# Performance work log

Hardware: AMD Instinct MI355X
Metric: run time of the kernel (lower is better)

Reference implementation:

```python
import jax, jax.numpy as jnp
import numpy as np

HIDDEN = 2048
HEADS = 16
HEAD_DIM = HIDDEN // HEADS          # 128
KV_RANK = HIDDEN // 8               # 256 (kv_compression_ratio = 8)
ATTN_DIM = HEADS * HEAD_DIM         # 2048
EPS = 1e-6


def setup_inputs() -> dict:
    key = jax.random.key(0)
    ks = jax.random.split(key, 6)
    B, L = 2, 2048
    x = jax.random.normal(ks[0], (B, L, HIDDEN), dtype=jnp.float32)
    # weights stored [in, out] (torch Linear applies x @ W.T; same math)
    s = lambda fan_in: 1.0 / np.sqrt(fan_in)
    Wq = jax.random.normal(ks[1], (HIDDEN, ATTN_DIM), dtype=jnp.float32) * s(HIDDEN)
    Wkv_down = jax.random.normal(ks[2], (HIDDEN, KV_RANK), dtype=jnp.float32) * s(HIDDEN)
    kv_norm_w = jnp.ones((KV_RANK,), dtype=jnp.float32)
    Wkv_up = jax.random.normal(ks[3], (KV_RANK, 2 * ATTN_DIM), dtype=jnp.float32) * s(KV_RANK)
    Wo = jax.random.normal(ks[4], (ATTN_DIM, HIDDEN), dtype=jnp.float32) * s(ATTN_DIM)
    return {"x": x, "Wq": Wq, "Wkv_down": Wkv_down, "kv_norm_w": kv_norm_w,
            "Wkv_up": Wkv_up, "Wo": Wo}


def rms_norm(x, w):
    ms = jnp.mean(x * x, axis=-1, keepdims=True)
    return w * (x * jax.lax.rsqrt(ms + EPS))


def reference(x, Wq, Wkv_down, kv_norm_w, Wkv_up, Wo):
    B, L, D = x.shape
    q = (x @ Wq).reshape(B, L, HEADS, HEAD_DIM)
    latent = rms_norm(x @ Wkv_down, kv_norm_w)            # [B, L, KV_RANK]
    kv = latent @ Wkv_up                                   # [B, L, 2*ATTN_DIM]
    k, v = jnp.split(kv, 2, axis=-1)
    k = k.reshape(B, L, HEADS, HEAD_DIM)
    v = v.reshape(B, L, HEADS, HEAD_DIM)
    scores = jnp.einsum('bxhd,byhd->bhxy', q, k) / np.sqrt(HEAD_DIM)
    causal = jnp.tril(jnp.ones((L, L), dtype=bool))
    scores = jnp.where(causal, scores, -jnp.inf)
    attn = jax.nn.softmax(scores, axis=-1)
    out = jnp.einsum('bhxy,byhd->bxhd', attn, v).reshape(B, L, ATTN_DIM)
    return out @ Wo
```

## Files before the change

kernel.cpp:

```cpp
#include <hip/hip_runtime.h>
#include <cstdint>
#include <cstddef>

typedef unsigned short u16;
typedef __bf16 bf16x8 __attribute__((ext_vector_type(8)));
typedef __bf16 bf16x2 __attribute__((ext_vector_type(2)));
typedef float f32x4 __attribute__((ext_vector_type(4)));

__device__ inline u16 f2bf(float f) {
  uint32_t u = __builtin_bit_cast(uint32_t, f);
  u += 0x7fffu + ((u >> 16) & 1u);
  return (u16)(u >> 16);
}

#if defined(__has_builtin)
#if __has_builtin(__builtin_amdgcn_cvt_pk_bf16_f32)
#define HAVE_PK_BF16 1
#endif
#endif

__device__ inline uint32_t pk2bf(float a, float b) {
#ifdef HAVE_PK_BF16
  bf16x2 v = __builtin_amdgcn_cvt_pk_bf16_f32(a, b);
  return __builtin_bit_cast(uint32_t, v);
#else
  return (uint32_t)f2bf(a) | ((uint32_t)f2bf(b) << 16);
#endif
}

__device__ inline f32x4 mfma16(bf16x8 a, bf16x8 b, f32x4 c) {
  return __builtin_amdgcn_mfma_f32_16x16x32_bf16(a, b, c, 0, 0, 0);
}

__device__ inline void gl_lds16(const u16* g, u16* l) {
  __builtin_amdgcn_global_load_lds(
      (const __attribute__((address_space(1))) uint32_t*)g,
      (__attribute__((address_space(3))) uint32_t*)l, 16, 0, 0);
}

__device__ void tcvt_dev(const float* __restrict__ in, u16* __restrict__ out,
                         int R, int C, int bx, int by, float (*t)[33], int tid) {
  int cb = bx * 32, rb = by * 32;
  int x = tid & 31, y = tid >> 5;
#pragma unroll
  for (int k = 0; k < 4; ++k)
    t[y + k * 8][x] = in[(size_t)(rb + y + k * 8) * C + cb + x];
  __syncthreads();
#pragma unroll
  for (int k = 0; k < 4; ++k)
    out[(size_t)(cb + y + k * 8) * R + rb + x] = f2bf(t[x][y + k * 8]);
}

__global__ __launch_bounds__(256) void k_prep(
    const float* __restrict__ x, const float* __restrict__ Wq,
    const float* __restrict__ Wkvd, const float* __restrict__ Wkvu,
    const float* __restrict__ Wo, u16* __restrict__ xbf,
    u16* __restrict__ WqkdT, u16* __restrict__ WkvuT, u16* __restrict__ WoT) {
  __shared__ float t[32][33];
  int bid = blockIdx.x, tid = threadIdx.x;
  if (bid < 8192) {
    int i = bid * 256 + tid;
    const float4 v = ((const float4*)x)[i];
    ushort4 o;
    o.x = f2bf(v.x); o.y = f2bf(v.y); o.z = f2bf(v.z); o.w = f2bf(v.w);
    ((ushort4*)xbf)[i] = o;
  } else if (bid < 12288) {
    int q = bid - 8192;
    tcvt_dev(Wq, WqkdT, 2048, 2048, q & 63, q >> 6, t, tid);
  } else if (bid < 12800) {
    int q = bid - 12288;
    tcvt_dev(Wkvd, WqkdT + 2048 * 2048, 2048, 256, q & 7, q >> 3, t, tid);
  } else if (bid < 13824) {
    int q = bid - 12800;
    tcvt_dev(Wkvu, WkvuT, 256, 4096, q & 127, q >> 7, t, tid);
  } else {
    int q = bid - 13824;
    tcvt_dev(Wo, WoT, 2048, 2048, q & 63, q >> 6, t, tid);
  }
}

__global__ __launch_bounds__(256) void k_rmsn(const u16* __restrict__ qc,
                                              const float* __restrict__ w,
                                              u16* __restrict__ out) {
  int row = blockIdx.x * 4 + (threadIdx.x >> 6);
  int lane = threadIdx.x & 63;
  const ushort4 u = *(const ushort4*)(qc + (size_t)row * 2304 + 2048 + lane * 4);
  float4 v;
  v.x = __builtin_bit_cast(float, (uint32_t)u.x << 16);
  v.y = __builtin_bit_cast(float, (uint32_t)u.y << 16);
  v.z = __builtin_bit_cast(float, (uint32_t)u.z << 16);
  v.w = __builtin_bit_cast(float, (uint32_t)u.w << 16);
  float ss = v.x * v.x + v.y * v.y + v.z * v.z + v.w * v.w;
#pragma unroll
  for (int off = 1; off < 64; off <<= 1) ss += __shfl_xor(ss, off);
  float r = rsqrtf(ss * (1.f / 256.f) + 1e-6f);
  const float4 wv = ((const float4*)w)[lane];
  ushort4 o;
  o.x = f2bf(v.x * r * wv.x);
  o.y = f2bf(v.y * r * wv.y);
  o.z = f2bf(v.z * r * wv.z);
  o.w = f2bf(v.w * r * wv.w);
  *(ushort4*)(out + (size_t)row * 256 + lane * 4) = o;
}

template <int BK, int MODE>
__global__ __launch_bounds__(256) void k_gemm(const u16* __restrict__ A,
                                              const u16* __restrict__ BT,
                                              void* __restrict__ C,
                                              u16* __restrict__ C2, int K,
                                              int ldc, float scale) {
  __shared__ __align__(16) u16 As[128 * BK];
  __shared__ __align__(16) u16 Bs[128 * BK];
  const int tid = threadIdx.x, wave = tid >> 6, lane = tid & 63;
  const int lanem = lane & 15, quad = lane >> 4;
  const int m0 = blockIdx.x * 128, n0 = blockIdx.y * 128;
  const int wr = wave >> 1, wc = wave & 1;
  f32x4 acc[4][4] = {};
  for (int k0 = 0; k0 < K; k0 += BK) {
    __syncthreads();
    if constexpr (BK == 32) {
      const int srow = lane >> 2, scol = (lane & 3) * 8;
#pragma unroll
      for (int c = 0; c < 2; ++c) {
        int p = wave * 2 + c;
        gl_lds16(A + (size_t)(m0 + p * 16 + srow) * K + k0 + scol, &As[p * 512]);
        gl_lds16(BT + (size_t)(n0 + p * 16 + srow) * K + k0 + scol, &Bs[p * 512]);
      }
    } else {
      const int srow = lane >> 3;
      const int scol = ((lane & 7) ^ srow) * 8;
#pragma unroll
      for (int c = 0; c < 4; ++c) {
        int p = wave * 4 + c;
        gl_lds16(A + (size_t)(m0 + p * 8 + srow) * K + k0 + scol, &As[p * 512]);
        gl_lds16(BT + (size_t)(n0 + p * 8 + srow) * K + k0 + scol, &Bs[p * 512]);
      }
    }
    __syncthreads();
#pragma unroll
    for (int kk = 0; kk < BK / 32; ++kk) {
      bf16x8 af[4], bff[4];
      if constexpr (BK == 32) {
#pragma unroll
        for (int i = 0; i < 4; ++i)
          af[i] = *(const bf16x8*)&As[(wr * 64 + i * 16 + lanem) * 32 + quad * 8];
#pragma unroll
        for (int j = 0; j < 4; ++j)
          bff[j] = *(const bf16x8*)&Bs[(wc * 64 + j * 16 + lanem) * 32 + quad * 8];
      } else {
        const int kp = ((kk * 4 + quad) ^ (lanem & 7)) << 3;
#pragma unroll
        for (int i = 0; i < 4; ++i)
          af[i] = *(const bf16x8*)&As[(wr * 64 + i * 16 + lanem) * 64 + kp];
#pragma unroll
        for (int j = 0; j < 4; ++j)
          bff[j] = *(const bf16x8*)&Bs[(wc * 64 + j * 16 + lanem) * 64 + kp];
      }
#pragma unroll
      for (int i = 0; i < 4; ++i)
#pragma unroll
        for (int j = 0; j < 4; ++j)
          acc[i][j] = mfma16(af[i], bff[j], acc[i][j]);
    }
  }
#pragma unroll
  for (int i = 0; i < 4; ++i)
#pragma unroll
    for (int j = 0; j < 4; ++j) {
      const int row0 = m0 + wr * 64 + i * 16 + quad * 4;
      const int col = n0 + wc * 64 + j * 16 + lanem;
      if constexpr (MODE == 2) {
        if (col >= 2048) {
          int cc = col - 2048, hh = cc >> 7, dd = cc & 127;
          int bb = row0 >> 11, ll = row0 & 2047;
          ushort4 pk;
          pk.x = f2bf(acc[i][j][0]);
          pk.y = f2bf(acc[i][j][1]);
          pk.z = f2bf(acc[i][j][2]);
          pk.w = f2bf(acc[i][j][3]);
          *(ushort4*)&C2[((size_t)(bb * 16 + hh) * 128 + dd) * 2048 + ll] = pk;
          continue;
        }
      }
#pragma unroll
      for (int r = 0; r < 4; ++r) {
        float v = acc[i][j][r] * scale;
        if constexpr (MODE == 0)
          ((float*)C)[(size_t)(row0 + r) * ldc + col] = v;
        else if constexpr (MODE == 1)
          ((u16*)C)[(size_t)(row0 + r) * ldc + col] = f2bf(v);
        else
          ((u16*)C)[(size_t)(row0 + r) * 2048 + col] = f2bf(v);
      }
    }
}

__global__ __launch_bounds__(256) void k_attn(const u16* __restrict__ qg,
                                              const u16* __restrict__ kg,
                                              const u16* __restrict__ vtg,
                                              u16* __restrict__ ao) {
  __shared__ __align__(16) u16 Ks[2][64 * 128];
  __shared__ __align__(16) u16 VTs[2][144 * 64];
  __shared__ __align__(16) u16 Ps[4][16 * 64];
  const int bid = blockIdx.x;
  const int p = bid >> 5, u = bid & 31;
  const int qt = (bid < 256) ? (15 - p) : (p - 8);
  const int bh = (u & 7) * 4 + (u >> 3);
  const int b = bh >> 4, h = bh & 15;
  const int tid = threadIdx.x, w = tid >> 6, lane = tid & 63;
  const int lanem = lane & 15, quad = lane >> 4;
  const int qb = qt * 128, nt = 2 * qt + 2;

  const int kr = lane >> 4, kc = lane & 15;
  const u16* kbp[4];
#pragma unroll
  for (int j = 0; j < 4; ++j) {
    int row = w * 16 + j * 4 + kr;
    kbp[j] = kg + (size_t)(b * 2048 + row) * 2048 + h * 128 +
             ((kc ^ (row & 15)) << 3);
  }
  const int vr = lane >> 3, vc = lane & 7;
  const u16* vbp[4];
#pragma unroll
  for (int j = 0; j < 4; ++j) {
    int row = w * 32 + j * 8 + vr;
    vbp[j] = vtg + (size_t)(bh * 128 + row) * 2048 + ((vc ^ vr) << 3);
  }

  bf16x8 qf[2][4];
#pragma unroll
  for (int g = 0; g < 2; ++g) {
    const u16* qp = qg +
                    (size_t)(b * 2048 + qb + w * 32 + g * 16 + lanem) * 2304 +
                    h * 128 + quad * 8;
#pragma unroll
    for (int c = 0; c < 4; ++c) qf[g][c] = *(const bf16x8*)(qp + c * 32);
  }
  f32x4 o[2][9] = {};

  int kpc[4], vposc[2], paddr[4][4];
#pragma unroll
  for (int c = 0; c < 4; ++c) kpc[c] = ((c * 4 + quad) ^ lanem) << 3;
#pragma unroll
  for (int kk = 0; kk < 2; ++kk)
    vposc[kk] = ((kk * 4 + quad) ^ (lanem & 7)) << 3;
#pragma unroll
  for (int ss = 0; ss < 4; ++ss) {
    const int g2 = ss * 2 + (lanem >> 3);
#pragma unroll
    for (int r = 0; r < 4; ++r) {
      const int row = quad * 4 + r;
      paddr[ss][r] = row * 64 + ((g2 ^ (row & 7)) << 3) + (lanem & 7);
    }
  }
  const int prd0 = lanem * 64 + ((quad ^ (lanem & 7)) << 3);
  const int prd1 = lanem * 64 + (((4 + quad) ^ (lanem & 7)) << 3);

#pragma unroll
  for (int j = 0; j < 4; ++j) gl_lds16(kbp[j], &Ks[0][(w * 16 + j * 4) * 128]);
#pragma unroll
  for (int j = 0; j < 4; ++j) gl_lds16(vbp[j], &VTs[0][(w * 32 + j * 8) * 64]);
#pragma unroll
  for (int j = 0; j < 4; ++j) { kbp[j] += 64 * 2048; vbp[j] += 64; }
  {
    const ushort4 ones4{0x3f80u, 0x3f80u, 0x3f80u, 0x3f80u};
    for (int i = tid; i < 512; i += 256) {
      int bufi = i >> 8, off = (i & 255) * 4;
      *(ushort4*)&VTs[bufi][128 * 64 + off] = ones4;
    }
  }

  for (int t = 0; t < nt; ++t) {
    __syncthreads();
    if (t + 1 < nt) {
      int nb = (t + 1) & 1;
#pragma unroll
      for (int j = 0; j < 4; ++j)
        gl_lds16(kbp[j], &Ks[nb][(w * 16 + j * 4) * 128]);
#pragma unroll
      for (int j = 0; j < 4; ++j)
        gl_lds16(vbp[j], &VTs[nb][(w * 32 + j * 8) * 64]);
#pragma unroll
      for (int j = 0; j < 4; ++j) { kbp[j] += 64 * 2048; vbp[j] += 64; }
    }
    const int buf = t & 1;
    const u16* ksb = &Ks[buf][lanem * 128];
    const u16* vsb = &VTs[buf][lanem * 64];
    f32x4 s[2][4] = {};
#pragma unroll
    for (int c = 0; c < 4; ++c) {
      const u16* ka = ksb + kpc[c];
#pragma unroll
      for (int ss = 0; ss < 4; ++ss) {
        bf16x8 kf = *(const bf16x8*)(ka + ss * 2048);
        s[0][ss] = mfma16(qf[0][c], kf, s[0][ss]);
        s[1][ss] = mfma16(qf[1][c], kf, s[1][ss]);
      }
    }
    if (t >= nt - 2) {
      const int krel = t * 64 - qb;
#pragma unroll
      for (int g = 0; g < 2; ++g) {
        const int row = w * 32 + g * 16 + quad * 4;
#pragma unroll
        for (int ss = 0; ss < 4; ++ss)
#pragma unroll
          for (int r = 0; r < 4; ++r)
            if (krel + ss * 16 + lanem > row + r) s[g][ss][r] = -1e30f;
      }
    }
    bf16x8 pf[2][2];
#pragma unroll
    for (int g = 0; g < 2; ++g) {
#pragma unroll
      for (int sp = 0; sp < 2; ++sp)
#pragma unroll
        for (int r = 0; r < 4; ++r) {
          uint32_t pk = pk2bf(exp2f(s[g][sp * 2][r]), exp2f(s[g][sp * 2 + 1][r]));
          Ps[w][paddr[sp * 2][r]] = (u16)pk;
          Ps[w][paddr[sp * 2 + 1][r]] = (u16)(pk >> 16);
        }
      pf[g][0] = *(const bf16x8*)&Ps[w][prd0];
      pf[g][1] = *(const bf16x8*)&Ps[w][prd1];
    }
#pragma unroll
    for (int dc = 0; dc < 9; ++dc) {
      const u16* va = vsb + dc * 1024;
      bf16x8 vf0 = *(const bf16x8*)(va + vposc[0]);
      bf16x8 vf1 = *(const bf16x8*)(va + vposc[1]);
      o[0][dc] = mfma16(pf[0][0], vf0, o[0][dc]);
      o[0][dc] = mfma16(pf[0][1], vf1, o[0][dc]);
      o[1][dc] = mfma16(pf[1][0], vf0, o[1][dc]);
      o[1][dc] = mfma16(pf[1][1], vf1, o[1][dc]);
    }
  }
#pragma unroll
  for (int g = 0; g < 2; ++g)
#pragma unroll
    for (int r = 0; r < 4; ++r) {
      const float inv = 1.f / o[g][8][r];
      u16* op = ao +
                (size_t)(b * 2048 + qb + w * 32 + g * 16 + quad * 4 + r) * 2048 +
                h * 128;
#pragma unroll
      for (int dc = 0; dc < 8; ++dc)
        op[dc * 16 + lanem] = f2bf(o[g][dc][r] * inv);
    }
}

extern "C" void kernel_launch(void* const* d_in, const int* in_sizes, int n_in,
                              void* d_out, int out_size, void* d_ws, size_t ws_size,
                              hipStream_t stream) {
  const float* x    = (const float*)d_in[0];
  const float* Wq   = (const float*)d_in[1];
  const float* Wkvd = (const float*)d_in[2];
  const float* wn   = (const float*)d_in[3];
  const float* Wkvu = (const float*)d_in[4];
  const float* Wo   = (const float*)d_in[5];
  float* out = (float*)d_out;

  char* w0 = (char*)d_ws;
  u16* xbf   = (u16*)(w0);
  u16* qc    = (u16*)(w0 + 16777216);
  u16* WqkdT = (u16*)(w0 + 35651584);
  u16* WoT   = (u16*)(w0 + 45088768);
  u16* WkvuT = (u16*)(w0 + 53477376);
  u16* kbf   = (u16*)(w0 + 55574528);
  u16* vtbf  = (u16*)(w0 + 72351744);
  u16* latbf = WqkdT;
  u16* aobf  = xbf;

  const float sc2 = 0.08838834764831845f * 1.4426950408889634f;

  k_prep<<<17920, 256, 0, stream>>>(x, Wq, Wkvd, Wkvu, Wo, xbf, WqkdT, WkvuT, WoT);
  k_gemm<32, 1><<<dim3(32, 18), 256, 0, stream>>>(xbf, WqkdT, qc, nullptr, 2048,
                                                  2304, sc2);
  k_rmsn<<<1024, 256, 0, stream>>>(qc, wn, latbf);
  k_gemm<64, 2><<<dim3(32, 32), 256, 0, stream>>>(latbf, WkvuT, kbf, vtbf, 256,
                                                  0, 1.0f);
  k_attn<<<512, 256, 0, stream>>>(qc, kbf, vtbf, aobf);
  k_gemm<32, 0><<<dim3(32, 16), 256, 0, stream>>>(aobf, WoT, out, nullptr, 2048,
                                                  2048, 1.0f);
}
```

Measured before the change: 327.1 us.

## Compute transposed S tiles to feed P directly from registers, drop LDS round-trip

After: 314.3 us. -3.9%, faster.

```diff
diff --git a/kernel.cpp b/kernel.cpp
--- a/kernel.cpp
+++ b/kernel.cpp
@@ -6,6 +6,7 @@
 typedef __bf16 bf16x8 __attribute__((ext_vector_type(8)));
 typedef __bf16 bf16x2 __attribute__((ext_vector_type(2)));
 typedef float f32x4 __attribute__((ext_vector_type(4)));
+typedef uint32_t u32x4 __attribute__((ext_vector_type(4)));
 
 __device__ inline u16 f2bf(float f) {
   uint32_t u = __builtin_bit_cast(uint32_t, f);
@@ -17,6 +18,12 @@
 #if __has_builtin(__builtin_amdgcn_cvt_pk_bf16_f32)
 #define HAVE_PK_BF16 1
 #endif
+#if __has_builtin(__builtin_amdgcn_exp2f)
+#define EXP2(x) __builtin_amdgcn_exp2f(x)
+#endif
+#endif
+#ifndef EXP2
+#define EXP2(x) exp2f(x)
 #endif
 
 __device__ inline uint32_t pk2bf(float a, float b) {
@@ -201,7 +208,6 @@
                                               u16* __restrict__ ao) {
   __shared__ __align__(16) u16 Ks[2][64 * 128];
   __shared__ __align__(16) u16 VTs[2][144 * 64];
-  __shared__ __align__(16) u16 Ps[4][16 * 64];
   const int bid = blockIdx.x;
   const int p = bid >> 5, u = bid & 31;
   const int qt = (bid < 256) ? (15 - p) : (p - 8);
@@ -215,9 +221,9 @@
   const u16* kbp[4];
 #pragma unroll
   for (int j = 0; j < 4; ++j) {
-    int row = w * 16 + j * 4 + kr;
-    kbp[j] = kg + (size_t)(b * 2048 + row) * 2048 + h * 128 +
-             ((kc ^ (row & 15)) << 3);
+    int key = ((w >> 1) << 5) + (j << 3) + ((w & 1) << 2) + kr;
+    kbp[j] = kg + (size_t)(b * 2048 + key) * 2048 + h * 128 +
+             ((kc ^ (j * 4 + kr)) << 3);
   }
   const int vr = lane >> 3, vc = lane & 7;
   const u16* vbp[4];
@@ -238,23 +244,12 @@
   }
   f32x4 o[2][9] = {};
 
-  int kpc[4], vposc[2], paddr[4][4];
+  int kpc[4], vposc[2];
 #pragma unroll
   for (int c = 0; c < 4; ++c) kpc[c] = ((c * 4 + quad) ^ lanem) << 3;
 #pragma unroll
   for (int kk = 0; kk < 2; ++kk)
     vposc[kk] = ((kk * 4 + quad) ^ (lanem & 7)) << 3;
-#pragma unroll
-  for (int ss = 0; ss < 4; ++ss) {
-    const int g2 = ss * 2 + (lanem >> 3);
-#pragma unroll
-    for (int r = 0; r < 4; ++r) {
-      const int row = quad * 4 + r;
-      paddr[ss][r] = row * 64 + ((g2 ^ (row & 7)) << 3) + (lanem & 7);
-    }
-  }
-  const int prd0 = lanem * 64 + ((quad ^ (lanem & 7)) << 3);
-  const int prd1 = lanem * 64 + (((4 + quad) ^ (lanem & 7)) << 3);
 
 #pragma unroll
   for (int j = 0; j < 4; ++j) gl_lds16(kbp[j], &Ks[0][(w * 16 + j * 4) * 128]);
@@ -293,36 +288,36 @@
 #pragma unroll
       for (int ss = 0; ss < 4; ++ss) {
         bf16x8 kf = *(const bf16x8*)(ka + ss * 2048);
-        s[0][ss] = mfma16(qf[0][c], kf, s[0][ss]);
-        s[1][ss] = mfma16(qf[1][c], kf, s[1][ss]);
+        s[0][ss] = mfma16(kf, qf[0][c], s[0][ss]);
+        s[1][ss] = mfma16(kf, qf[1][c], s[1][ss]);
       }
     }
     if (t >= nt - 2) {
       const int krel = t * 64 - qb;
 #pragma unroll
       for (int g = 0; g < 2; ++g) {
-        const int row = w * 32 + g * 16 + quad * 4;
-#pragma unroll
-        for (int ss = 0; ss < 4; ++ss)
+        const int qrow = w * 32 + g * 16 + lanem;
+#pragma unroll
+        for (int ss = 0; ss < 4; ++ss) {
+          const int kb0 = krel + ((ss & 2) << 4) + ((ss & 1) << 2) + (quad << 3);
 #pragma unroll
           for (int r = 0; r < 4; ++r)
-            if (krel + ss * 16 + lanem > row + r) s[g][ss][r] = -1e30f;
+            if (kb0 + r > qrow) s[g][ss][r] = -1e30f;
+        }
       }
     }
     bf16x8 pf[2][2];
 #pragma unroll
-    for (int g = 0; g < 2; ++g) {
-#pragma unroll
-      for (int sp = 0; sp < 2; ++sp)
-#pragma unroll
-        for (int r = 0; r < 4; ++r) {
-          uint32_t pk = pk2bf(exp2f(s[g][sp * 2][r]), exp2f(s[g][sp * 2 + 1][r]));
-          Ps[w][paddr[sp * 2][r]] = (u16)pk;
-          Ps[w][paddr[sp * 2 + 1][r]] = (u16)(pk >> 16);
-        }
-      pf[g][0] = *(const bf16x8*)&Ps[w][prd0];
-      pf[g][1] = *(const bf16x8*)&Ps[w][prd1];
-    }
+    for (int g = 0; g < 2; ++g)
+#pragma unroll
+      for (int f = 0; f < 2; ++f) {
+        u32x4 pw;
+        pw.x = pk2bf(EXP2(s[g][2 * f][0]), EXP2(s[g][2 * f][1]));
+        pw.y = pk2bf(EXP2(s[g][2 * f][2]), EXP2(s[g][2 * f][3]));
+        pw.z = pk2bf(EXP2(s[g][2 * f + 1][0]), EXP2(s[g][2 * f + 1][1]));
+        pw.w = pk2bf(EXP2(s[g][2 * f + 1][2]), EXP2(s[g][2 * f + 1][3]));
+        pf[g][f] = __builtin_bit_cast(bf16x8, pw);
+      }
 #pragma unroll
     for (int dc = 0; dc < 9; ++dc) {
       const u16* va = vsb + dc * 1024;
```
